# Performance work log

Hardware: AMD Instinct MI355X
Metric: run time of the kernel (lower is better)

## Reference

```python
import jax, jax.numpy as jnp
import numpy as np

# Module config (matches init_kwargs)
B, H, W, C = 8, 32, 32, 512
NH = 8                      # num_heads
D = C // NH                 # per-head qkv channels (downsize_factor = num_heads)
HO = 512 // NH              # head_output_channels = output_channels // num_heads
COUT = 512                  # output_channels (== C so shortcut works)
EPS = 1e-3                  # keras BatchNormalization default epsilon


def setup_inputs() -> dict:
    key = jax.random.key(0)
    ks = jax.random.split(key, 10)
    s_in = C ** -0.5
    return {
        "x": jax.random.normal(ks[0], (B, H, W, C), jnp.float32),
        # 1x1 convs == per-head matmuls, no bias (use_bias=False)
        "Wk": jax.random.normal(ks[1], (NH, C, D), jnp.float32) * s_in,
        "Wq": jax.random.normal(ks[2], (NH, C, D), jnp.float32) * s_in,
        "Wv": jax.random.normal(ks[3], (NH, C, D), jnp.float32) * s_in,
        "Wo_head": jax.random.normal(ks[4], (NH, D, HO), jnp.float32) * (D ** -0.5),
        # per-head BatchNorm (inference: moving statistics)
        "gamma": jnp.ones((NH, HO), jnp.float32),
        "beta": jnp.zeros((NH, HO), jnp.float32),
        "mov_mean": jnp.zeros((NH, HO), jnp.float32),
        "mov_var": jnp.ones((NH, HO), jnp.float32),
        # relative position embeddings, init stddev = channels**-0.5
        "rel_w": jax.random.normal(ks[5], (NH, 2 * W - 1, D), jnp.float32) * s_in,
        "rel_h": jax.random.normal(ks[6], (NH, 2 * H - 1, D), jnp.float32) * s_in,
        # final 1x1 conv over concatenated heads
        "Wout": jax.random.normal(ks[7], (NH * HO, COUT), jnp.float32) * ((NH * HO) ** -0.5),
    }


def rel_to_abs(x):
    # x: [b, nh, L, 2L-1] relative logits -> [b, nh, L, L] absolute logits
    b, nh, L, _ = x.shape
    x = jnp.pad(x, ((0, 0), (0, 0), (0, 0), (0, 1)))        # [b,nh,L,2L]
    flat = x.reshape(b, nh, L * 2 * L)
    flat = jnp.pad(flat, ((0, 0), (0, 0), (0, L - 1)))       # [b,nh,2L^2+L-1]
    final = flat.reshape(b, nh, L + 1, 2 * L - 1)
    return final[:, :, :L, L - 1:]


def reference(x, Wk, Wq, Wv, Wo_head, gamma, beta, mov_mean, mov_var, rel_w, rel_h, Wout):
    b, h, w, c = x.shape
    n = h * w
    xf = x.reshape(b, n, c)
    # per-head 1x1 conv projections -> [b, nh, n, d]
    k = jnp.einsum('bnc,hcd->bhnd', xf, Wk)
    q = jnp.einsum('bnc,hcd->bhnd', xf, Wq)
    v = jnp.einsum('bnc,hcd->bhnd', xf, Wv)
    # Keras Dot(axes=2)([key, query]): rows index key positions, cols query positions
    scores = jnp.einsum('bhid,bhjd->bhij', k, q)             # [b,nh,n,n]
    # relative position logits computed from q (spatial mode)
    q5 = q.reshape(b, NH, h, w, D)
    wl = jnp.einsum('bhxyd,hmd->bhxym', q5, rel_w)           # [b,nh,H,W,2W-1]
    w_abs = rel_to_abs(wl.reshape(b * NH, h, w, 2 * w - 1)).reshape(b, NH, h, w, w)
    hl = jnp.einsum('bhxyd,hmd->bhyxm', q5, rel_h)           # [b,nh,W,H,2H-1] (q transposed x<->y)
    h_abs = rel_to_abs(hl.reshape(b * NH, w, h, 2 * h - 1)).reshape(b, NH, w, h, h)
    h_abs = h_abs.transpose(0, 1, 3, 2, 4)                   # [b,nh,x,y,x2]
    # logits[(x,y),(x2,y2)] = w_abs[x,y,y2] + h_abs[x,y,x2]
    s6 = scores.reshape(b, NH, h, w, h, w)
    s6 = s6 + w_abs[:, :, :, :, None, :] + h_abs[:, :, :, :, :, None]
    attn = jax.nn.softmax(s6.reshape(b, NH, n, n), axis=-1)
    out = jnp.einsum('bhij,bhjd->bhid', attn, v)             # [b,nh,n,d]
    ho = jnp.einsum('bhid,hde->bhie', out, Wo_head)          # per-head output 1x1 conv
    # per-head BatchNorm (inference)
    ho = gamma[None, :, None, :] * (ho - mov_mean[None, :, None, :]) * \
         jax.lax.rsqrt(mov_var[None, :, None, :] + EPS) + beta[None, :, None, :]
    cat = ho.transpose(0, 2, 1, 3).reshape(b, n, NH * HO)    # channel concat of heads
    y = (cat @ Wout).reshape(b, h, w, COUT)                  # final 1x1 conv
    return y + x                                             # shortcut connection
```

## Files before the change

### kernel.cpp

```cpp
#include <hip/hip_runtime.h>
#include <stdint.h>

typedef unsigned short u16;
typedef __attribute__((ext_vector_type(8))) short short8;
typedef __attribute__((ext_vector_type(4))) float f32x4;
typedef __attribute__((ext_vector_type(16))) float f32x16;
typedef __attribute__((ext_vector_type(4))) unsigned short us4;
typedef __attribute__((ext_vector_type(4))) uint32_t u32x4;
typedef __attribute__((ext_vector_type(2))) int i32x2;
typedef __attribute__((ext_vector_type(4))) int i32x4;

#define MFMA(a,b,c)   __builtin_amdgcn_mfma_f32_16x16x32_bf16((a),(b),(c),0,0,0)
#define MFMA32(a,b,c) __builtin_amdgcn_mfma_f32_32x32x16_bf16((a),(b),(c),0,0,0)
#define L2E 1.44269504f

__device__ __forceinline__ u16 f2bf(float f){
    union { float f; uint32_t i; } v; v.f = f;
    uint32_t u = v.i;
    return (u16)((u + 0x7fffu + ((u >> 16) & 1u)) >> 16);
}
__device__ __forceinline__ uint32_t cvtpk(float lo, float hi){
    uint32_t r;
    asm("v_cvt_pk_bf16_f32 %0, %1, %2" : "=v"(r) : "v"(lo), "v"(hi));
    return r;
}
__device__ __forceinline__ void barrier_lgkm(){
    __builtin_amdgcn_sched_barrier(0);
    asm volatile("s_waitcnt lgkmcnt(0)" ::: "memory");
    __builtin_amdgcn_s_barrier();
    __builtin_amdgcn_sched_barrier(0);
}

#define WS_W1T    0u
#define WS_WOT    1572864u
#define WS_WOUTT  1638400u
#define WS_RELW   2162688u
#define WS_RELH   2227200u
#define WS_SCALE  2291712u
#define WS_SHIFT  2293760u
#define WS_Q      10684416u
#define WS_K      19073024u
#define WS_VT     27461632u
#define WS_RW     35850240u
#define WS_RH     44238848u
#define WS_Z      52627456u

__global__ __launch_bounds__(256) void k0_setup(
    const float* Wk, const float* Wq, const float* Wv, const float* Wo,
    const float* gamma, const float* beta, const float* mean, const float* var,
    const float* relw, const float* relh, const float* Wout,
    u16* W1T, u16* WoT, u16* WoutT,
    u16* RWbf, u16* RHbf, float* scaleZ, float* shiftZ)
{
    int idx = blockIdx.x * 256 + threadIdx.x;
    if (idx < 786432) {
        int co = idx >> 9, c = idx & 511;
        int p = co >> 9, rem = co & 511;
        int h = rem >> 6, d = rem & 63;
        const float* src = (p == 0) ? Wq : (p == 1) ? Wk : Wv;
        W1T[idx] = f2bf(src[h * 32768 + c * 64 + d]);
    } else if (idx < 819200) {
        int r = idx - 786432;
        int h = r >> 12; int e = (r & 4095) >> 6, ep = r & 63;
        WoT[h * 4096 + ep * 64 + e] = f2bf(Wo[h * 4096 + e * 64 + ep]);
    } else if (idx < 1081344) {
        int r = idx - 819200;
        int c = r >> 9, co = r & 511;
        WoutT[co * 512 + c] = f2bf(Wout[c * 512 + co]);
    } else if (idx < 1145856) {
        int r = idx - 1081344;
        if (r < 32256) RWbf[r] = f2bf(relw[r]);
        else           RHbf[r - 32256] = f2bf(relh[r - 32256]);
    } else if (idx < 1146368) {
        int ch = idx - 1145856;
        float sc = gamma[ch] * rsqrtf(var[ch] + 1e-3f);
        scaleZ[ch] = sc;
        shiftZ[ch] = beta[ch] - mean[ch] * sc;
    }
}

__device__ __forceinline__ void packA(u16* dst, f32x4 a0, f32x4 a1, f32x4 a2, f32x4 a3){
    u32x4 v0 = { cvtpk(a0.x,a0.y), cvtpk(a0.z,a0.w), cvtpk(a1.x,a1.y), cvtpk(a1.z,a1.w) };
    u32x4 v1 = { cvtpk(a2.x,a2.y), cvtpk(a2.z,a2.w), cvtpk(a3.x,a3.y), cvtpk(a3.z,a3.w) };
    *(u32x4*)dst = v0;
    *(u32x4*)(dst + 8) = v1;
}

__global__ __launch_bounds__(256, 3) void k1_gemm(
    const float* __restrict__ Xf, const u16* __restrict__ W1T,
    u16* Q, u16* K, u16* Vt)
{
    int s = blockIdx.x;
    int xcd = s & 7, r8 = s >> 3;
    int nt = r8 % 12, mt = (r8 / 12) * 8 + xcd;
    int tid = threadIdx.x;
    int w = tid >> 6, l = tid & 63, lg = l >> 4, ll = l & 15;
    int wm = w >> 1, wn = w & 1;
    int i0 = mt * 128, co0 = nt * 128;

    __shared__ __align__(16) u16 SM[20480];
    u16* As = SM;
    u16* Bs = SM + 10240;

    int row = tid >> 1, c16 = (tid & 1) * 16;
    int st = row * 40 + c16;
    const float* ArowF = Xf + (size_t)(i0 + row) * 512 + c16;
    const u16*   Brow  = W1T + (size_t)(co0 + row) * 512 + c16;

    f32x4 acc[4][4];
#pragma unroll
    for (int m = 0; m < 4; m++)
#pragma unroll
        for (int nn = 0; nn < 4; nn++) acc[m][nn] = (f32x4){0,0,0,0};

    f32x4 ra0 = *(const f32x4*)&ArowF[0];
    f32x4 ra1 = *(const f32x4*)&ArowF[4];
    f32x4 ra2 = *(const f32x4*)&ArowF[8];
    f32x4 ra3 = *(const f32x4*)&ArowF[12];
    short8 rb0 = *(const short8*)&Brow[0];
    short8 rb1 = *(const short8*)&Brow[8];
    packA(&As[st], ra0, ra1, ra2, ra3);
    *(short8*)&Bs[st] = rb0; *(short8*)&Bs[st + 8] = rb1;
    __syncthreads();
    for (int ks = 0; ks < 16; ++ks) {
        int cur = ks & 1, nxt = cur ^ 1;
        if (ks < 15) {
            ra0 = *(const f32x4*)&ArowF[(ks + 1) * 32];
            ra1 = *(const f32x4*)&ArowF[(ks + 1) * 32 + 4];
            ra2 = *(const f32x4*)&ArowF[(ks + 1) * 32 + 8];
            ra3 = *(const f32x4*)&ArowF[(ks + 1) * 32 + 12];
            rb0 = *(const short8*)&Brow[(ks + 1) * 32];
            rb1 = *(const short8*)&Brow[(ks + 1) * 32 + 8];
        }
        const u16* Ab = As + cur * 5120;
        const u16* Bb = Bs + cur * 5120;
        short8 af[4], bfr[4];
#pragma unroll
        for (int m = 0; m < 4; m++)
            af[m] = *(const short8*)&Ab[(wm * 64 + m * 16 + ll) * 40 + lg * 8];
#pragma unroll
        for (int nn = 0; nn < 4; nn++)
            bfr[nn] = *(const short8*)&Bb[(wn * 64 + nn * 16 + ll) * 40 + lg * 8];
#pragma unroll
        for (int m = 0; m < 4; m++)
#pragma unroll
            for (int nn = 0; nn < 4; nn++)
                acc[m][nn] = MFMA(af[m], bfr[nn], acc[m][nn]);
        if (ks < 15) {
            int so = nxt * 5120 + st;
            packA(&As[so], ra0, ra1, ra2, ra3);
            *(short8*)&Bs[so] = rb0; *(short8*)&Bs[so + 8] = rb1;
        }
        __syncthreads();
    }

    int b = mt >> 3, nloc0 = (mt & 7) * 128;
    u16* Ts = SM;
    if (nt < 8) {
        u16* dst = (nt < 4) ? Q : K;
        float qsc = (nt < 4) ? L2E : 1.0f;
        int coB = (nt & 3) * 128;
#pragma unroll
        for (int nn = 0; nn < 4; nn++)
#pragma unroll
            for (int m = 0; m < 4; m++)
#pragma unroll
                for (int r = 0; r < 4; r++)
                    Ts[(wm * 64 + m * 16 + lg * 4 + r) * 136 + wn * 64 + nn * 16 + ll]
                        = f2bf(acc[m][nn][r] * qsc);
        __syncthreads();
        int chunk = tid & 7;
#pragma unroll
        for (int j = 0; j < 8; j++) {
            int vr = j * 32 + (tid >> 3);
            int irow = vr >> 1, half = vr & 1;
            int hh = (coB >> 6) + half;
            u16* qdst = dst + ((size_t)(b * 8 + hh) * 1024 + nloc0 + irow) * 64;
            *(short8*)&qdst[chunk * 8] = *(const short8*)&Ts[irow * 136 + half * 64 + chunk * 8];
        }
    } else {
#pragma unroll
        for (int nn = 0; nn < 4; nn++)
#pragma unroll
            for (int m = 0; m < 4; m++)
#pragma unroll
                for (int r = 0; r < 4; r++)
                    Ts[(wn * 64 + nn * 16 + ll) * 136 + wm * 64 + m * 16 + lg * 4 + r]
                        = f2bf(acc[m][nn][r]);
        __syncthreads();
        int co_l = tid >> 1, half = tid & 1;
        int co = (nt - 8) * 128 + co_l;
        int hh = (co >> 6) & 7, d = co & 63;
        u16* vdst = Vt + ((size_t)(b * 8 + hh) * 64 + d) * 1024 + nloc0 + half * 64;
#pragma unroll
        for (int j = 0; j < 8; j++)
            *(short8*)&vdst[j * 8] = *(const short8*)&Ts[co_l * 136 + half * 64 + j * 8];
    }
}

__global__ __launch_bounds__(256) void k1b_rel(
    const u16* Q, const u16* relw, const u16* relh,
    float* rw_abs, float* rh_abs)
{
    int bid = blockIdx.x;
    int it = bid & 15, bh = bid >> 4, h = bh & 7;
    int tid = threadIdx.x;
    int w = tid >> 6, l = tid & 63, lg = l >> 4, ll = l & 15;
    int i0 = it * 64;

    __shared__ float wls[64 * 66];
    __shared__ float hls[64 * 66];

    const u16* qb = Q + ((size_t)bh * 1024 + i0 + w * 16) * 64;
    short8 a0 = *(const short8*)&qb[ll * 64 + lg * 8];
    short8 a1 = *(const short8*)&qb[ll * 64 + 32 + lg * 8];
    const u16* rwb = relw + h * 4032;
    const u16* rhb = relh + h * 4032;

#pragma unroll
    for (int mt = 0; mt < 4; ++mt) {
        int m = mt * 16 + ll; if (m > 62) m = 62;
        f32x4 aw = (f32x4){0,0,0,0}, ah = (f32x4){0,0,0,0};
        short8 w0 = *(const short8*)&rwb[m * 64 + lg * 8];
        short8 w1 = *(const short8*)&rwb[m * 64 + 32 + lg * 8];
        aw = MFMA(a0, w0, aw); aw = MFMA(a1, w1, aw);
        short8 h0 = *(const short8*)&rhb[m * 64 + lg * 8];
        short8 h1 = *(const short8*)&rhb[m * 64 + 32 + lg * 8];
        ah = MFMA(a0, h0, ah); ah = MFMA(a1, h1, ah);
#pragma unroll
        for (int r = 0; r < 4; r++) {
            int il = w * 16 + lg * 4 + r;
            wls[il * 66 + mt * 16 + ll] = aw[r];
            hls[il * 66 + mt * 16 + ll] = ah[r];
        }
    }
    __syncthreads();
    {
        int il = tid >> 2, c0 = (tid & 3) * 8;
        int i = i0 + il, y = i & 31, x = i >> 5;
        float* ro = rw_abs + ((size_t)bh * 1024 + i) * 32 + c0;
        float* ho = rh_abs + ((size_t)bh * 1024 + i) * 32 + c0;
#pragma unroll
        for (int c = 0; c < 8; c++) {
            ro[c] = wls[il * 66 + (c0 + c) - y + 31];
            ho[c] = hls[il * 66 + (c0 + c) - x + 31];
        }
    }
}

__global__ __launch_bounds__(256, 2) void k2_attn(
    const u16* Q, const u16* K, const u16* Vt,
    const float* rw_abs, const float* rh_abs,
    const u16* WoT, const float* scaleZ, const float* shiftZ,
    u16* Z)
{
    int s_ = blockIdx.x;
    int xcd = s_ & 7, r8 = s_ >> 3;
    int it = r8 & 7, bh = (r8 >> 3) * 8 + xcd;
    int b = bh >> 3, h = bh & 7;
    int tid = threadIdx.x;
    int wv = tid >> 6, l = tid & 63, il = l & 31, hf = l >> 5;
    int i0 = it * 128;
    int iw = i0 + wv * 32;
    int i_lane = iw + il;

    __shared__ __align__(16) char smem[53760];
    u16*   Qs  = (u16*)smem;
    u16*   Vs  = (u16*)(smem + 18432);
    float* rhS = (float*)(smem + 36864);

    const u16* kb = K + ((size_t)bh * 1024 + iw) * 64;
    short8 kf0 = *(const short8*)&kb[il * 64 + hf * 8];
    short8 kf1 = *(const short8*)&kb[il * 64 + 16 + hf * 8];
    short8 kf2 = *(const short8*)&kb[il * 64 + 32 + hf * 8];
    short8 kf3 = *(const short8*)&kb[il * 64 + 48 + hf * 8];

    const float* rwb = rw_abs + ((size_t)bh * 1024 + i_lane) * 32;
    float rw16[16];
#pragma unroll
    for (int reg = 0; reg < 16; reg++)
        rw16[reg] = rwb[(reg & 3) + 8 * (reg >> 2) + 4 * hf];

    {
        int il2 = tid >> 1, c0 = (tid & 1) * 16;
        const float* src = rh_abs + ((size_t)bh * 1024 + i0 + il2) * 32 + c0;
#pragma unroll
        for (int c = 0; c < 16; c++) rhS[il2 * 33 + c0 + c] = src[c];
    }

    f32x16 o0, o1;
#pragma unroll
    for (int reg = 0; reg < 16; reg++) { o0[reg] = 0.f; o1[reg] = 0.f; }
    float lsum = 0.f;

    const u16* qg = Q + (size_t)bh * 65536;
    const u16* vg = Vt + (size_t)bh * 65536;
    int srow = tid >> 2, sg = (tid & 3) * 8;

    short8 pq0 = *(const short8*)&qg[(size_t)srow * 64 + sg];
    short8 pq1 = *(const short8*)&qg[(size_t)srow * 64 + sg + 32];
    short8 pv0 = *(const short8*)&vg[(size_t)srow * 1024 + sg];
    short8 pv1 = *(const short8*)&vg[(size_t)srow * 1024 + sg + 32];
    *(short8*)&Qs[srow * 72 + sg] = pq0;
    *(short8*)&Qs[srow * 72 + sg + 32] = pq1;
    *(short8*)&Vs[srow * 72 + sg] = pv0;
    *(short8*)&Vs[srow * 72 + sg + 32] = pv1;
    pq0 = *(const short8*)&qg[(size_t)(64 + srow) * 64 + sg];
    pq1 = *(const short8*)&qg[(size_t)(64 + srow) * 64 + sg + 32];
    pv0 = *(const short8*)&vg[(size_t)srow * 1024 + 64 + sg];
    pv1 = *(const short8*)&vg[(size_t)srow * 1024 + 64 + sg + 32];

    for (int ch = 0; ch < 16; ++ch) {
        int cur = ch & 1, nxt = cur ^ 1;
        barrier_lgkm();
        if (ch < 15) {
            *(short8*)&Qs[nxt * 4608 + srow * 72 + sg] = pq0;
            *(short8*)&Qs[nxt * 4608 + srow * 72 + sg + 32] = pq1;
            *(short8*)&Vs[nxt * 4608 + srow * 72 + sg] = pv0;
            *(short8*)&Vs[nxt * 4608 + srow * 72 + sg + 32] = pv1;
        }
        if (ch < 14) {
            int j2 = (ch + 2) * 64;
            pq0 = *(const short8*)&qg[(size_t)(j2 + srow) * 64 + sg];
            pq1 = *(const short8*)&qg[(size_t)(j2 + srow) * 64 + sg + 32];
            pv0 = *(const short8*)&vg[(size_t)srow * 1024 + j2 + sg];
            pv1 = *(const short8*)&vg[(size_t)srow * 1024 + j2 + sg + 32];
        }
        const u16* Qb = Qs + cur * 4608;
        const u16* Vb = Vs + cur * 4608;

#pragma unroll
        for (int u = 0; u < 2; ++u) {
            int jl = u * 32;
            float rhv = rhS[(wv * 32 + il) * 33 + ch * 2 + u];
            f32x16 sA;
#pragma unroll
            for (int reg = 0; reg < 16; reg++) sA[reg] = rw16[reg] + rhv;
            short8 aq0 = *(const short8*)&Qb[(jl + il) * 72 + hf * 8];
            short8 aq1 = *(const short8*)&Qb[(jl + il) * 72 + 16 + hf * 8];
            short8 aq2 = *(const short8*)&Qb[(jl + il) * 72 + 32 + hf * 8];
            short8 aq3 = *(const short8*)&Qb[(jl + il) * 72 + 48 + hf * 8];
            sA = MFMA32(aq0, kf0, sA);
            sA = MFMA32(aq1, kf1, sA);
            sA = MFMA32(aq2, kf2, sA);
            sA = MFMA32(aq3, kf3, sA);

            float p[16];
#pragma unroll
            for (int reg = 0; reg < 16; reg++) p[reg] = __builtin_amdgcn_exp2f(sA[reg]);
            {
                float t0 = (p[0] + p[1]) + (p[2] + p[3]);
                float t1 = (p[4] + p[5]) + (p[6] + p[7]);
                float t2 = (p[8] + p[9]) + (p[10] + p[11]);
                float t3 = (p[12] + p[13]) + (p[14] + p[15]);
                lsum += (t0 + t1) + (t2 + t3);
            }
            uint32_t W[8];
#pragma unroll
            for (int q = 0; q < 4; q++) {
                W[q * 2]     = cvtpk(p[q * 4 + 0], p[q * 4 + 1]);
                W[q * 2 + 1] = cvtpk(p[q * 4 + 2], p[q * 4 + 3]);
            }
            short8 pf0, pf1;
            {
                i32x2 rA = __builtin_amdgcn_permlane32_swap((int)W[0], (int)W[2], false, false);
                i32x2 rB = __builtin_amdgcn_permlane32_swap((int)W[1], (int)W[3], false, false);
                i32x4 t = { rA.x, rB.x, rA.y, rB.y };
                pf0 = *(short8*)&t;
            }
            {
                i32x2 rA = __builtin_amdgcn_permlane32_swap((int)W[4], (int)W[6], false, false);
                i32x2 rB = __builtin_amdgcn_permlane32_swap((int)W[5], (int)W[7], false, false);
                i32x4 t = { rA.x, rB.x, rA.y, rB.y };
                pf1 = *(short8*)&t;
            }

            __builtin_amdgcn_s_setprio(1);
            short8 av;
            av = *(const short8*)&Vb[il * 72 + jl + hf * 8];
            o0 = MFMA32(av, pf0, o0);
            av = *(const short8*)&Vb[(32 + il) * 72 + jl + hf * 8];
            o1 = MFMA32(av, pf0, o1);
            av = *(const short8*)&Vb[il * 72 + jl + 16 + hf * 8];
            o0 = MFMA32(av, pf1, o0);
            av = *(const short8*)&Vb[(32 + il) * 72 + jl + 16 + hf * 8];
            o1 = MFMA32(av, pf1, o1);
            __builtin_amdgcn_s_setprio(0);
        }
    }

    lsum += __shfl_xor(lsum, 32);
    float inv = 1.0f / lsum;
    __syncthreads();

    u16* Ob = (u16*)smem + wv * 2304;
#pragma unroll
    for (int q = 0; q < 4; q++) {
        uint32_t w0 = cvtpk(o0[q * 4 + 0] * inv, o0[q * 4 + 1] * inv);
        uint32_t w1 = cvtpk(o0[q * 4 + 2] * inv, o0[q * 4 + 3] * inv);
        *(uint32_t*)&Ob[il * 72 + q * 8 + hf * 4]     = w0;
        *(uint32_t*)&Ob[il * 72 + q * 8 + hf * 4 + 2] = w1;
        uint32_t w2 = cvtpk(o1[q * 4 + 0] * inv, o1[q * 4 + 1] * inv);
        uint32_t w3 = cvtpk(o1[q * 4 + 2] * inv, o1[q * 4 + 3] * inv);
        *(uint32_t*)&Ob[il * 72 + 32 + q * 8 + hf * 4]     = w2;
        *(uint32_t*)&Ob[il * 72 + 32 + q * 8 + hf * 4 + 2] = w3;
    }
    short8 ao0 = *(const short8*)&Ob[il * 72 + hf * 8];
    short8 ao1 = *(const short8*)&Ob[il * 72 + 16 + hf * 8];
    short8 ao2 = *(const short8*)&Ob[il * 72 + 32 + hf * 8];
    short8 ao3 = *(const short8*)&Ob[il * 72 + 48 + hf * 8];

    const u16* wob = WoT + h * 4096;
#pragma unroll
    for (int et = 0; et < 2; et++) {
        short8 bo0 = *(const short8*)&wob[(et * 32 + il) * 64 + hf * 8];
        short8 bo1 = *(const short8*)&wob[(et * 32 + il) * 64 + 16 + hf * 8];
        short8 bo2 = *(const short8*)&wob[(et * 32 + il) * 64 + 32 + hf * 8];
        short8 bo3 = *(const short8*)&wob[(et * 32 + il) * 64 + 48 + hf * 8];
        f32x16 zacc;
#pragma unroll
        for (int reg = 0; reg < 16; reg++) zacc[reg] = 0.f;
        zacc = MFMA32(ao0, bo0, zacc);
        zacc = MFMA32(ao1, bo1, zacc);
        zacc = MFMA32(ao2, bo2, zacc);
        zacc = MFMA32(ao3, bo3, zacc);
        int chn = h * 64 + et * 32 + il;
        float scv = scaleZ[chn], shv = shiftZ[chn];
#pragma unroll
        for (int reg = 0; reg < 16; reg++) {
            int i = iw + (reg & 3) + 8 * (reg >> 2) + 4 * hf;
            Z[((size_t)(b * 1024) + i) * 512 + chn] = f2bf(zacc[reg] * scv + shv);
        }
    }
}

__global__ __launch_bounds__(256, 4) void k3_gemm(
    const u16* __restrict__ Zb, const u16* __restrict__ WoutT,
    const float* __restrict__ X, float* Y)
{
    int s = blockIdx.x;
    int xcd = s & 7, r8 = s >> 3;
    int nt = r8 & 7, mt = (r8 >> 3) * 8 + xcd;
    int tid = threadIdx.x;
    int w = tid >> 6, l = tid & 63, lg = l >> 4, ll = l & 15;
    int wm = w >> 1, wn = w & 1;
    int i0 = mt * 64, co0 = nt * 64;

    __shared__ __align__(16) u16 SM[10240];
    u16* As = SM;
    u16* Bs = SM + 5120;

    int row = tid >> 2, c8 = (tid & 3) * 8;
    int st = row * 40 + c8;
    const u16* Arow = Zb + (size_t)(i0 + row) * 512 + c8;
    const u16* Brow = WoutT + (size_t)(co0 + row) * 512 + c8;

    f32x4 acc[2][2];
#pragma unroll
    for (int m = 0; m < 2; m++)
#pragma unroll
        for (int nn = 0; nn < 2; nn++) acc[m][nn] = (f32x4){0,0,0,0};

    short8 ra = *(const short8*)&Arow[0];
    short8 rb = *(const short8*)&Brow[0];
    *(short8*)&As[st] = ra;
    *(short8*)&Bs[st] = rb;
    __syncthreads();
    for (int ks = 0; ks < 16; ++ks) {
        int cur = ks & 1, nxt = cur ^ 1;
        if (ks < 15) {
            ra = *(const short8*)&Arow[(ks + 1) * 32];
            rb = *(const short8*)&Brow[(ks + 1) * 32];
        }
        const u16* Ab = As + cur * 2560;
        const u16* Bb = Bs + cur * 2560;
        short8 af[2], bfr[2];
#pragma unroll
        for (int m = 0; m < 2; m++)
            af[m] = *(const short8*)&Ab[(wm * 32 + m * 16 + ll) * 40 + lg * 8];
#pragma unroll
        for (int nn = 0; nn < 2; nn++)
            bfr[nn] = *(const short8*)&Bb[(wn * 32 + nn * 16 + ll) * 40 + lg * 8];
#pragma unroll
        for (int m = 0; m < 2; m++)
#pragma unroll
            for (int nn = 0; nn < 2; nn++)
                acc[m][nn] = MFMA(af[m], bfr[nn], acc[m][nn]);
        if (ks < 15) {
            int so = nxt * 2560 + st;
            *(short8*)&As[so] = ra;
            *(short8*)&Bs[so] = rb;
        }
        __syncthreads();
    }

#pragma unroll
    for (int m = 0; m < 2; m++)
#pragma unroll
        for (int nn = 0; nn < 2; nn++) {
            int i = i0 + wm * 32 + m * 16 + lg * 4;
            int co = co0 + wn * 32 + nn * 16 + ll;
#pragma unroll
            for (int r = 0; r < 4; r++) {
                size_t idx = (size_t)(i + r) * 512 + co;
                Y[idx] = acc[m][nn][r] + X[idx];
            }
        }
}

extern "C" void kernel_launch(void* const* d_in, const int* in_sizes, int n_in,
                              void* d_out, int out_size, void* d_ws, size_t ws_size,
                              hipStream_t stream)
{
    const float* x     = (const float*)d_in[0];
    const float* Wk    = (const float*)d_in[1];
    const float* Wq    = (const float*)d_in[2];
    const float* Wv    = (const float*)d_in[3];
    const float* Wo    = (const float*)d_in[4];
    const float* gamma = (const float*)d_in[5];
    const float* beta  = (const float*)d_in[6];
    const float* mmean = (const float*)d_in[7];
    const float* mvar  = (const float*)d_in[8];
    const float* relw  = (const float*)d_in[9];
    const float* relh  = (const float*)d_in[10];
    const float* Wout  = (const float*)d_in[11];

    char* ws = (char*)d_ws;
    u16*   W1T    = (u16*)(ws + WS_W1T);
    u16*   WoT    = (u16*)(ws + WS_WOT);
    u16*   WoutT  = (u16*)(ws + WS_WOUTT);
    u16*   RWbf   = (u16*)(ws + WS_RELW);
    u16*   RHbf   = (u16*)(ws + WS_RELH);
    float* scaleZ = (float*)(ws + WS_SCALE);
    float* shiftZ = (float*)(ws + WS_SHIFT);
    u16*   Qw     = (u16*)(ws + WS_Q);
    u16*   Kw     = (u16*)(ws + WS_K);
    u16*   Vtw    = (u16*)(ws + WS_VT);
    float* rw     = (float*)(ws + WS_RW);
    float* rh     = (float*)(ws + WS_RH);
    u16*   Zw     = (u16*)(ws + WS_Z);

    k0_setup<<<4478, 256, 0, stream>>>(Wk, Wq, Wv, Wo, gamma, beta, mmean, mvar,
                                       relw, relh, Wout,
                                       W1T, WoT, WoutT, RWbf, RHbf,
                                       scaleZ, shiftZ);
    k1_gemm<<<768, 256, 0, stream>>>(x, W1T, Qw, Kw, Vtw);
    k1b_rel<<<1024, 256, 0, stream>>>(Qw, RWbf, RHbf, rw, rh);
    k2_attn<<<512, 256, 0, stream>>>(Qw, Kw, Vtw, rw, rh, WoT, scaleZ, shiftZ, Zw);
    k3_gemm<<<1024, 256, 0, stream>>>(Zw, WoutT, x, (float*)d_out);
}
```

Baseline: 101.8 us.

## Fuse relative-position logit computation into the attention kernel

Removes the separate k1b_rel kernel, which computed the relative width and height logits with MFMA and stored them as fp32 rw_abs and rh_abs buffers in global memory. k2_attn now loads its own Q rows and the bf16 relative embeddings, computes the logits with 32x32 MFMAs, and does the rel-to-abs diagonal shift through per-wave shared-memory scratch before the main loop. This drops one kernel launch and a large fp32 global write and re-read. The cost is extra MFMA work, shared-memory traffic and an added barrier in the prologue of the attention kernel, which may raise register pressure.

```diff
diff --git a/kernel.cpp b/kernel.cpp
--- a/kernel.cpp
+++ b/kernel.cpp
@@ -41,8 +41,6 @@
 #define WS_Q      10684416u
 #define WS_K      19073024u
 #define WS_VT     27461632u
-#define WS_RW     35850240u
-#define WS_RH     44238848u
 #define WS_Z      52627456u
 
 __global__ __launch_bounds__(256) void k0_setup(
@@ -198,59 +196,9 @@
     }
 }
 
-__global__ __launch_bounds__(256) void k1b_rel(
-    const u16* Q, const u16* relw, const u16* relh,
-    float* rw_abs, float* rh_abs)
-{
-    int bid = blockIdx.x;
-    int it = bid & 15, bh = bid >> 4, h = bh & 7;
-    int tid = threadIdx.x;
-    int w = tid >> 6, l = tid & 63, lg = l >> 4, ll = l & 15;
-    int i0 = it * 64;
-
-    __shared__ float wls[64 * 66];
-    __shared__ float hls[64 * 66];
-
-    const u16* qb = Q + ((size_t)bh * 1024 + i0 + w * 16) * 64;
-    short8 a0 = *(const short8*)&qb[ll * 64 + lg * 8];
-    short8 a1 = *(const short8*)&qb[ll * 64 + 32 + lg * 8];
-    const u16* rwb = relw + h * 4032;
-    const u16* rhb = relh + h * 4032;
-
-#pragma unroll
-    for (int mt = 0; mt < 4; ++mt) {
-        int m = mt * 16 + ll; if (m > 62) m = 62;
-        f32x4 aw = (f32x4){0,0,0,0}, ah = (f32x4){0,0,0,0};
-        short8 w0 = *(const short8*)&rwb[m * 64 + lg * 8];
-        short8 w1 = *(const short8*)&rwb[m * 64 + 32 + lg * 8];
-        aw = MFMA(a0, w0, aw); aw = MFMA(a1, w1, aw);
-        short8 h0 = *(const short8*)&rhb[m * 64 + lg * 8];
-        short8 h1 = *(const short8*)&rhb[m * 64 + 32 + lg * 8];
-        ah = MFMA(a0, h0, ah); ah = MFMA(a1, h1, ah);
-#pragma unroll
-        for (int r = 0; r < 4; r++) {
-            int il = w * 16 + lg * 4 + r;
-            wls[il * 66 + mt * 16 + ll] = aw[r];
-            hls[il * 66 + mt * 16 + ll] = ah[r];
-        }
-    }
-    __syncthreads();
-    {
-        int il = tid >> 2, c0 = (tid & 3) * 8;
-        int i = i0 + il, y = i & 31, x = i >> 5;
-        float* ro = rw_abs + ((size_t)bh * 1024 + i) * 32 + c0;
-        float* ho = rh_abs + ((size_t)bh * 1024 + i) * 32 + c0;
-#pragma unroll
-        for (int c = 0; c < 8; c++) {
-            ro[c] = wls[il * 66 + (c0 + c) - y + 31];
-            ho[c] = hls[il * 66 + (c0 + c) - x + 31];
-        }
-    }
-}
-
 __global__ __launch_bounds__(256, 2) void k2_attn(
     const u16* Q, const u16* K, const u16* Vt,
-    const float* rw_abs, const float* rh_abs,
+    const u16* relwb, const u16* relhb,
     const u16* WoT, const float* scaleZ, const float* shiftZ,
     u16* Z)
 {
@@ -262,7 +210,6 @@
     int wv = tid >> 6, l = tid & 63, il = l & 31, hf = l >> 5;
     int i0 = it * 128;
     int iw = i0 + wv * 32;
-    int i_lane = iw + il;
 
     __shared__ __align__(16) char smem[53760];
     u16*   Qs  = (u16*)smem;
@@ -275,18 +222,66 @@
     short8 kf2 = *(const short8*)&kb[il * 64 + 32 + hf * 8];
     short8 kf3 = *(const short8*)&kb[il * 64 + 48 + hf * 8];
 
-    const float* rwb = rw_abs + ((size_t)bh * 1024 + i_lane) * 32;
     float rw16[16];
-#pragma unroll
-    for (int reg = 0; reg < 16; reg++)
-        rw16[reg] = rwb[(reg & 3) + 8 * (reg >> 2) + 4 * hf];
-
     {
-        int il2 = tid >> 1, c0 = (tid & 1) * 16;
-        const float* src = rh_abs + ((size_t)bh * 1024 + i0 + il2) * 32 + c0;
-#pragma unroll
-        for (int c = 0; c < 16; c++) rhS[il2 * 33 + c0 + c] = src[c];
-    }
+        float* wlb = (float*)(smem + wv * 8448);
+        const u16* qsrc = Q + ((size_t)bh * 1024 + iw) * 64;
+        short8 qa0 = *(const short8*)&qsrc[il * 64 + hf * 8];
+        short8 qa1 = *(const short8*)&qsrc[il * 64 + 16 + hf * 8];
+        short8 qa2 = *(const short8*)&qsrc[il * 64 + 32 + hf * 8];
+        short8 qa3 = *(const short8*)&qsrc[il * 64 + 48 + hf * 8];
+        int m1 = (32 + il > 62) ? 62 : 32 + il;
+        const u16* rwsrc = relwb + h * 4032;
+        const u16* rhsrc = relhb + h * 4032;
+#pragma unroll
+        for (int mt2 = 0; mt2 < 2; mt2++) {
+            int m = mt2 ? m1 : il;
+            short8 b0 = *(const short8*)&rwsrc[m * 64 + hf * 8];
+            short8 b1 = *(const short8*)&rwsrc[m * 64 + 16 + hf * 8];
+            short8 b2 = *(const short8*)&rwsrc[m * 64 + 32 + hf * 8];
+            short8 b3 = *(const short8*)&rwsrc[m * 64 + 48 + hf * 8];
+            f32x16 wa;
+#pragma unroll
+            for (int reg = 0; reg < 16; reg++) wa[reg] = 0.f;
+            wa = MFMA32(qa0, b0, wa);
+            wa = MFMA32(qa1, b1, wa);
+            wa = MFMA32(qa2, b2, wa);
+            wa = MFMA32(qa3, b3, wa);
+#pragma unroll
+            for (int reg = 0; reg < 16; reg++)
+                wlb[((reg & 3) + 8 * (reg >> 2) + 4 * hf) * 66 + mt2 * 32 + il] = wa[reg];
+        }
+#pragma unroll
+        for (int reg = 0; reg < 16; reg++) {
+            int c = (reg & 3) + 8 * (reg >> 2) + 4 * hf;
+            rw16[reg] = wlb[il * 65 + c + 31];
+        }
+#pragma unroll
+        for (int mt2 = 0; mt2 < 2; mt2++) {
+            int m = mt2 ? m1 : il;
+            short8 b0 = *(const short8*)&rhsrc[m * 64 + hf * 8];
+            short8 b1 = *(const short8*)&rhsrc[m * 64 + 16 + hf * 8];
+            short8 b2 = *(const short8*)&rhsrc[m * 64 + 32 + hf * 8];
+            short8 b3 = *(const short8*)&rhsrc[m * 64 + 48 + hf * 8];
+            f32x16 ha;
+#pragma unroll
+            for (int reg = 0; reg < 16; reg++) ha[reg] = 0.f;
+            ha = MFMA32(qa0, b0, ha);
+            ha = MFMA32(qa1, b1, ha);
+            ha = MFMA32(qa2, b2, ha);
+            ha = MFMA32(qa3, b3, ha);
+#pragma unroll
+            for (int reg = 0; reg < 16; reg++)
+                wlb[((reg & 3) + 8 * (reg >> 2) + 4 * hf) * 66 + mt2 * 32 + il] = ha[reg];
+        }
+        int x = iw >> 5;
+#pragma unroll
+        for (int reg = 0; reg < 16; reg++) {
+            int c = (reg & 3) + 8 * (reg >> 2) + 4 * hf;
+            rhS[(wv * 32 + il) * 33 + c] = wlb[il * 66 + c + 31 - x];
+        }
+    }
+    __syncthreads();
 
     f32x16 o0, o1;
 #pragma unroll
@@ -536,8 +531,6 @@
     u16*   Qw     = (u16*)(ws + WS_Q);
     u16*   Kw     = (u16*)(ws + WS_K);
     u16*   Vtw    = (u16*)(ws + WS_VT);
-    float* rw     = (float*)(ws + WS_RW);
-    float* rh     = (float*)(ws + WS_RH);
     u16*   Zw     = (u16*)(ws + WS_Z);
 
     k0_setup<<<4478, 256, 0, stream>>>(Wk, Wq, Wv, Wo, gamma, beta, mmean, mvar,
@@ -545,7 +538,6 @@
                                        W1T, WoT, WoutT, RWbf, RHbf,
                                        scaleZ, shiftZ);
     k1_gemm<<<768, 256, 0, stream>>>(x, W1T, Qw, Kw, Vtw);
-    k1b_rel<<<1024, 256, 0, stream>>>(Qw, RWbf, RHbf, rw, rh);
-    k2_attn<<<512, 256, 0, stream>>>(Qw, Kw, Vtw, rw, rh, WoT, scaleZ, shiftZ, Zw);
+    k2_attn<<<512, 256, 0, stream>>>(Qw, Kw, Vtw, RWbf, RHbf, WoT, scaleZ, shiftZ, Zw);
     k3_gemm<<<1024, 256, 0, stream>>>(Zw, WoutT, x, (float*)d_out);
 }
```

Result: faster. 85.59 us, median of 2 (-16.0%).
